# Performance work log

Hardware: AMD Instinct MI355X
Metric: run time of the kernel (lower is better)

Reference implementation:

```python
import jax, jax.numpy as jnp
import numpy as np

GRID_SIZE = 5
SPLINE_ORDER = 3
HIDDEN = 128
N = 131072
K = 256          # num_cluster
EPS = 1e-8       # torch.cosine_similarity eps
N_COEF = GRID_SIZE + SPLINE_ORDER  # 8 spline basis functions per input feature


def make_grid():
    # efficient-kan grid: grid_range [-1,1], extended by spline_order on each side
    h = 2.0 / GRID_SIZE
    g = jnp.arange(-SPLINE_ORDER, GRID_SIZE + SPLINE_ORDER + 1, dtype=jnp.float32) * h - 1.0
    return jnp.tile(g[None, :], (HIDDEN, 1))  # (in, grid_size + 2*order + 1) = (128, 12)


def b_splines(x, grid):
    # x: (N, in), grid: (in, G) -> bases: (N, in, grid_size + spline_order)
    xe = x[..., None]
    bases = ((xe >= grid[:, :-1]) & (xe < grid[:, 1:])).astype(x.dtype)
    for p in range(1, SPLINE_ORDER + 1):
        left = (xe - grid[:, :-(p + 1)]) / (grid[:, p:-1] - grid[:, :-(p + 1)])
        right = (grid[:, p + 1:] - xe) / (grid[:, p + 1:] - grid[:, 1:-p])
        bases = left * bases[..., :-1] + right * bases[..., 1:]
    return bases


def kan_linear(x, grid, base_w, spline_w, scaler):
    # efficient-kan KANLinear: base path + spline path
    base = jax.nn.silu(x) @ base_w.T                       # (N, out)
    sp = b_splines(x, grid)                                # (N, in, coef)
    sw = spline_w * scaler[..., None]                      # (out, in, coef)
    return base + jnp.einsum('nic,oic->no', sp, sw)


def setup_inputs() -> dict:
    key = jax.random.key(0)
    ks = jax.random.split(key, 9)
    s = 1.0 / np.sqrt(HIDDEN)
    return {
        'x': jax.random.normal(ks[0], (N, HIDDEN), jnp.float32),
        'prototypes': jax.random.normal(ks[1], (K, HIDDEN), jnp.float32),
        'grid': make_grid(),
        'base_w1': jax.random.normal(ks[2], (HIDDEN, HIDDEN), jnp.float32) * s,
        'spline_w1': jax.random.normal(ks[3], (HIDDEN, HIDDEN, N_COEF), jnp.float32) * 0.1,
        'scaler1': jax.random.normal(ks[4], (HIDDEN, HIDDEN), jnp.float32) * s + 1.0,
        'base_w2': jax.random.normal(ks[5], (HIDDEN, HIDDEN), jnp.float32) * s,
        'spline_w2': jax.random.normal(ks[6], (HIDDEN, HIDDEN, N_COEF), jnp.float32) * 0.1,
        'scaler2': jax.random.normal(ks[7], (HIDDEN, HIDDEN), jnp.float32) * s + 1.0,
    }


def reference(x, prototypes, grid, base_w1, spline_w1, scaler1, base_w2, spline_w2, scaler2):
    # KAN([128,128,128]) = two KANLinear layers
    h = kan_linear(x, grid, base_w1, spline_w1, scaler1)
    emb = kan_linear(h, grid, base_w2, spline_w2, scaler2)     # (N, 128)
    # cosine similarity to all prototypes = normalized matmul (same math as
    # the broadcasted torch.cosine_similarity, without the (N,K,H) intermediate)
    xn = emb / jnp.maximum(jnp.linalg.norm(emb, axis=-1, keepdims=True), EPS)
    pn = prototypes / jnp.maximum(jnp.linalg.norm(prototypes, axis=-1, keepdims=True), EPS)
    sim = xn @ pn.T                                            # (N, K)
    cluster_assignments = jnp.argmax(sim, axis=1)              # (N,)
    return emb, cluster_assignments
```

## Files before the change

kernel.cpp:

```cpp
#include <hip/hip_runtime.h>
#include <math.h>

typedef unsigned short u16;
typedef _Float16 f16;
typedef __attribute__((ext_vector_type(8))) _Float16 f16x8;
typedef __attribute__((ext_vector_type(4))) float f32x4;

#define N_ROWS 131072
#define HID 128
#define WS_CH 8192
#define N_WCH 72
#define N_PCH 8

__device__ __forceinline__ void f16_split(float v, f16& hi, f16& lo) {
    f16 h = (f16)v;
    hi = h;
    lo = (f16)(v - (float)h);
}

__device__ __forceinline__ void spline8(float xv, float* a8) {
    float s  = (xv + 2.2f) * 2.5f;
    float tf = floorf(s);
    int   tt = (int)tf;
    bool valid = (tt >= 0) && (tt <= 10);
    float kt = (float)(tt - 3) * 0.4f - 1.0f;
    float u  = (xv - kt) * 2.5f;
    float u2 = u * u, u3 = u2 * u;
    float om = 1.0f - u;
    float b3 = u3 * (1.0f / 6.0f);
    float b2 = (-3.f * u3 + 3.f * u2 + 3.f * u + 1.f) * (1.0f / 6.0f);
    float b1 = (3.f * u3 - 6.f * u2 + 4.f) * (1.0f / 6.0f);
    float b0 = om * om * om * (1.0f / 6.0f);
    #pragma unroll
    for (int c = 0; c < 8; ++c) {
        int d = tt - c;
        float v = 0.f;
        v = (d == 0) ? b3 : v;
        v = (d == 1) ? b2 : v;
        v = (d == 2) ? b1 : v;
        v = (d == 3) ? b0 : v;
        a8[c] = valid ? v : 0.f;
    }
}

#define GLOAD_LDS16(g, l)                                                         \
    __builtin_amdgcn_global_load_lds(                                             \
        (const __attribute__((address_space(1))) unsigned int*)(g),               \
        (__attribute__((address_space(3))) unsigned int*)(l), 16, 0, 0)

__global__ __launch_bounds__(256)
void pack_weights(const float* __restrict__ bw1, const float* __restrict__ sw1,
                  const float* __restrict__ sc1,
                  const float* __restrict__ bw2, const float* __restrict__ sw2,
                  const float* __restrict__ sc2,
                  const float* __restrict__ protos, u16* __restrict__ ws)
{
    int gid = blockIdx.x * 256 + threadIdx.x;
    if (gid < N_WCH * 4096) {
        int l  = gid / (36 * 4096);
        int r  = gid % (36 * 4096);
        int ch = r / 4096;
        int e  = r % 4096;
        int o  = e >> 5;
        int kl = e & 31;
        const float* bw = l ? bw2 : bw1;
        const float* sw = l ? sw2 : sw1;
        const float* sc = l ? sc2 : sc1;
        float v;
        if (ch < 4) {
            v = bw[o * HID + ch * 32 + kl];
        } else {
            int i = (ch - 4) * 4 + (kl >> 3);
            v = sw[(o * HID + i) * 8 + (kl & 7)] * sc[o * HID + i];
        }
        f16 hi, lo; f16_split(v, hi, lo);
        int nt = o >> 4, n = o & 15, kq = kl >> 3, c = kl & 7;
        size_t base = (size_t)(l * 36 + ch) * WS_CH;
        size_t idx  = ((size_t)nt * 64 + kq * 16 + n) * 8 + c;
        ws[base + idx]        = __builtin_bit_cast(u16, hi);
        ws[base + 4096 + idx] = __builtin_bit_cast(u16, lo);
    } else if (gid < (N_WCH + N_PCH) * 4096) {
        int r  = gid - N_WCH * 4096;
        int hk = r / 4096;
        int e  = r % 4096;
        int pl = e >> 5;
        int kl = e & 31;
        int half = hk >> 2, kc = hk & 3;
        float v = protos[(size_t)(half * 128 + pl) * HID + kc * 32 + kl];
        f16 hi, lo; f16_split(v, hi, lo);
        int nt = pl >> 4, n = pl & 15, kq = kl >> 3, c = kl & 7;
        size_t base = (size_t)(N_WCH + hk) * WS_CH;
        size_t idx  = ((size_t)nt * 64 + kq * 16 + n) * 8 + c;
        ws[base + idx]        = __builtin_bit_cast(u16, hi);
        ws[base + 4096 + idx] = __builtin_bit_cast(u16, lo);
    }
}

__global__ __launch_bounds__(256, 3)
void kan_fused(const float* __restrict__ x, const float* __restrict__ protos,
               const u16* __restrict__ wpack,
               float* __restrict__ emb_out, float* __restrict__ assign_out)
{
    __shared__ float t[64][132];
    __shared__ u16   Bfrag[2][8][64][8];
    __shared__ float rnp[256];

    const int tid  = threadIdx.x;
    const int lane = tid & 63;
    const int w    = tid >> 6;
    const int m    = lane & 15;
    const int q    = lane >> 4;
    const int row  = w * 16 + m;
    const int brow = blockIdx.x * 64;

    {
        const float4* pr = (const float4*)(protos + (size_t)tid * HID);
        float s = 0.0f;
        #pragma unroll
        for (int j = 0; j < 32; ++j) {
            float4 v = pr[j];
            s += v.x * v.x + v.y * v.y + v.z * v.z + v.w * v.w;
        }
        rnp[tid] = 1.0f / fmaxf(sqrtf(s), 1e-8f);
    }

    {
        const int m2 = tid >> 2, kq2 = tid & 3;
        const float4* src = (const float4*)(x + (size_t)(brow + m2) * HID + kq2 * 32);
        #pragma unroll
        for (int j = 0; j < 8; ++j) {
            float4 v = src[j];
            int k = kq2 * 32 + j * 4;
            t[m2][k] = v.x; t[m2][k + 1] = v.y; t[m2][k + 2] = v.z; t[m2][k + 3] = v.w;
        }
    }
    __syncthreads();

    union { f16x8 v; f16 h[8]; } ah, al, bh, bl;
    f32x4 acc[8];

    for (int l = 0; l < 2; ++l) {
        #pragma unroll
        for (int nt = 0; nt < 8; ++nt) acc[nt] = (f32x4){0.f, 0.f, 0.f, 0.f};

        for (int ch = 0; ch < 36; ++ch) {
            float a8[8];
            if (ch < 4) {
                #pragma unroll
                for (int j = 0; j < 8; ++j) {
                    float xv = t[row][ch * 32 + q * 8 + j];
                    a8[j] = xv / (1.0f + expf(-xv));
                }
            } else {
                spline8(t[row][(ch - 4) * 4 + q], a8);
            }
            #pragma unroll
            for (int j = 0; j < 8; ++j) f16_split(a8[j], ah.h[j], al.h[j]);

            __syncthreads();
            {
                const char* gsrc = (const char*)(wpack + (size_t)(l * 36 + ch) * WS_CH);
                char* lbase = (char*)&Bfrag[0][0][0][0] + w * 4096;
                #pragma unroll
                for (int i = 0; i < 4; ++i)
                    GLOAD_LDS16(gsrc + w * 4096 + i * 1024 + (size_t)lane * 16,
                                lbase + i * 1024);
            }
            __syncthreads();

            #pragma unroll
            for (int nt = 0; nt < 8; ++nt) {
                bh.v = *(const f16x8*)Bfrag[0][nt][lane];
                bl.v = *(const f16x8*)Bfrag[1][nt][lane];
                acc[nt] = __builtin_amdgcn_mfma_f32_16x16x32_f16(ah.v, bh.v, acc[nt], 0, 0, 0);
                acc[nt] = __builtin_amdgcn_mfma_f32_16x16x32_f16(ah.v, bl.v, acc[nt], 0, 0, 0);
                acc[nt] = __builtin_amdgcn_mfma_f32_16x16x32_f16(al.v, bh.v, acc[nt], 0, 0, 0);
                acc[nt] = __builtin_amdgcn_mfma_f32_16x16x32_f16(al.v, bl.v, acc[nt], 0, 0, 0);
            }
        }

        #pragma unroll
        for (int nt = 0; nt < 8; ++nt)
            #pragma unroll
            for (int r = 0; r < 4; ++r)
                t[w * 16 + q * 4 + r][nt * 16 + m] = acc[nt][r];
        __syncthreads();
    }

    {
        const int m2 = tid >> 2, kq2 = tid & 3;
        float* dst = emb_out + (size_t)(brow + m2) * HID + kq2 * 32;
        #pragma unroll
        for (int j = 0; j < 8; ++j)
            *(float4*)(dst + j * 4) = *(const float4*)&t[m2][kq2 * 32 + j * 4];
    }

    float best[4]; int bi[4];
    #pragma unroll
    for (int r = 0; r < 4; ++r) { best[r] = -3.402823466e+38f; bi[r] = 0; }

    for (int half = 0; half < 2; ++half) {
        #pragma unroll
        for (int nt = 0; nt < 8; ++nt) acc[nt] = (f32x4){0.f, 0.f, 0.f, 0.f};

        for (int kc = 0; kc < 4; ++kc) {
            float a8[8];
            #pragma unroll
            for (int j = 0; j < 8; ++j) a8[j] = t[row][kc * 32 + q * 8 + j];
            #pragma unroll
            for (int j = 0; j < 8; ++j) f16_split(a8[j], ah.h[j], al.h[j]);

            __syncthreads();
            {
                const char* gsrc =
                    (const char*)(wpack + (size_t)(N_WCH + half * 4 + kc) * WS_CH);
                char* lbase = (char*)&Bfrag[0][0][0][0] + w * 4096;
                #pragma unroll
                for (int i = 0; i < 4; ++i)
                    GLOAD_LDS16(gsrc + w * 4096 + i * 1024 + (size_t)lane * 16,
                                lbase + i * 1024);
            }
            __syncthreads();

            #pragma unroll
            for (int nt = 0; nt < 8; ++nt) {
                bh.v = *(const f16x8*)Bfrag[0][nt][lane];
                bl.v = *(const f16x8*)Bfrag[1][nt][lane];
                acc[nt] = __builtin_amdgcn_mfma_f32_16x16x32_f16(ah.v, bh.v, acc[nt], 0, 0, 0);
                acc[nt] = __builtin_amdgcn_mfma_f32_16x16x32_f16(ah.v, bl.v, acc[nt], 0, 0, 0);
                acc[nt] = __builtin_amdgcn_mfma_f32_16x16x32_f16(al.v, bh.v, acc[nt], 0, 0, 0);
                acc[nt] = __builtin_amdgcn_mfma_f32_16x16x32_f16(al.v, bl.v, acc[nt], 0, 0, 0);
            }
        }

        #pragma unroll
        for (int nt = 0; nt < 8; ++nt) {
            int p = half * 128 + nt * 16 + m;
            float rp = rnp[p];
            #pragma unroll
            for (int r = 0; r < 4; ++r) {
                float v = acc[nt][r] * rp;
                if (v > best[r]) { best[r] = v; bi[r] = p; }
            }
        }
    }

    #pragma unroll
    for (int r = 0; r < 4; ++r) {
        #pragma unroll
        for (int off = 1; off < 16; off <<= 1) {
            float ov = __shfl_xor(best[r], off);
            int   oi = __shfl_xor(bi[r], off);
            if (ov > best[r] || (ov == best[r] && oi < bi[r])) { best[r] = ov; bi[r] = oi; }
        }
        if (m == 0)
            assign_out[(size_t)brow + w * 16 + q * 4 + r] = (float)bi[r];
    }
}

extern "C" void kernel_launch(void* const* d_in, const int* in_sizes, int n_in,
                              void* d_out, int out_size, void* d_ws, size_t ws_size,
                              hipStream_t stream) {
    (void)in_sizes; (void)n_in; (void)out_size; (void)ws_size;

    const float* x      = (const float*)d_in[0];
    const float* protos = (const float*)d_in[1];
    const float* bw1 = (const float*)d_in[3];
    const float* sw1 = (const float*)d_in[4];
    const float* sc1 = (const float*)d_in[5];
    const float* bw2 = (const float*)d_in[6];
    const float* sw2 = (const float*)d_in[7];
    const float* sc2 = (const float*)d_in[8];

    float* out    = (float*)d_out;
    float* embp   = out;
    float* assign = out + (size_t)N_ROWS * HID;
    u16*   wpack  = (u16*)d_ws;

    pack_weights<<<dim3((N_WCH + N_PCH) * 4096 / 256), dim3(256), 0, stream>>>(
        bw1, sw1, sc1, bw2, sw2, sc2, protos, wpack);
    kan_fused<<<dim3(N_ROWS / 64), dim3(256), 0, stream>>>(
        x, protos, wpack, embp, assign);
}
```

Baseline: 468.7 us.

## Load weight fragments directly from global into registers, drop LDS staging and barriers

```diff
diff --git a/kernel.cpp b/kernel.cpp
--- a/kernel.cpp
+++ b/kernel.cpp
@@ -42,11 +42,6 @@
         a8[c] = valid ? v : 0.f;
     }
 }
-
-#define GLOAD_LDS16(g, l)                                                         \
-    __builtin_amdgcn_global_load_lds(                                             \
-        (const __attribute__((address_space(1))) unsigned int*)(g),               \
-        (__attribute__((address_space(3))) unsigned int*)(l), 16, 0, 0)
 
 __global__ __launch_bounds__(256)
 void pack_weights(const float* __restrict__ bw1, const float* __restrict__ sw1,
@@ -96,13 +91,12 @@
     }
 }
 
-__global__ __launch_bounds__(256, 3)
+__global__ __launch_bounds__(256, 2)
 void kan_fused(const float* __restrict__ x, const float* __restrict__ protos,
                const u16* __restrict__ wpack,
                float* __restrict__ emb_out, float* __restrict__ assign_out)
 {
     __shared__ float t[64][132];
-    __shared__ u16   Bfrag[2][8][64][8];
     __shared__ float rnp[256];
 
     const int tid  = threadIdx.x;
@@ -125,18 +119,19 @@
     }
 
     {
-        const int m2 = tid >> 2, kq2 = tid & 3;
-        const float4* src = (const float4*)(x + (size_t)(brow + m2) * HID + kq2 * 32);
+        const int rl = w * 16 + (lane >> 2);
+        const int kq2 = lane & 3;
+        const float4* src = (const float4*)(x + (size_t)(brow + rl) * HID + kq2 * 32);
         #pragma unroll
         for (int j = 0; j < 8; ++j) {
             float4 v = src[j];
             int k = kq2 * 32 + j * 4;
-            t[m2][k] = v.x; t[m2][k + 1] = v.y; t[m2][k + 2] = v.z; t[m2][k + 3] = v.w;
+            t[rl][k] = v.x; t[rl][k + 1] = v.y; t[rl][k + 2] = v.z; t[rl][k + 3] = v.w;
         }
     }
     __syncthreads();
 
-    union { f16x8 v; f16 h[8]; } ah, al, bh, bl;
+    union { f16x8 v; f16 h[8]; } ah, al;
     f32x4 acc[8];
 
     for (int l = 0; l < 2; ++l) {
@@ -146,36 +141,27 @@
         for (int ch = 0; ch < 36; ++ch) {
             float a8[8];
             if (ch < 4) {
+                float4 xv0 = *(const float4*)&t[row][ch * 32 + q * 8];
+                float4 xv1 = *(const float4*)&t[row][ch * 32 + q * 8 + 4];
+                float xs[8] = { xv0.x, xv0.y, xv0.z, xv0.w, xv1.x, xv1.y, xv1.z, xv1.w };
                 #pragma unroll
-                for (int j = 0; j < 8; ++j) {
-                    float xv = t[row][ch * 32 + q * 8 + j];
-                    a8[j] = xv / (1.0f + expf(-xv));
-                }
+                for (int j = 0; j < 8; ++j)
+                    a8[j] = xs[j] / (1.0f + __expf(-xs[j]));
             } else {
                 spline8(t[row][(ch - 4) * 4 + q], a8);
             }
             #pragma unroll
             for (int j = 0; j < 8; ++j) f16_split(a8[j], ah.h[j], al.h[j]);
 
-            __syncthreads();
-            {
-                const char* gsrc = (const char*)(wpack + (size_t)(l * 36 + ch) * WS_CH);
-                char* lbase = (char*)&Bfrag[0][0][0][0] + w * 4096;
-                #pragma unroll
-                for (int i = 0; i < 4; ++i)
-                    GLOAD_LDS16(gsrc + w * 4096 + i * 1024 + (size_t)lane * 16,
-                                lbase + i * 1024);
-            }
-            __syncthreads();
-
+            const u16* cb = wpack + (size_t)(l * 36 + ch) * WS_CH + (size_t)lane * 8;
             #pragma unroll
             for (int nt = 0; nt < 8; ++nt) {
-                bh.v = *(const f16x8*)Bfrag[0][nt][lane];
-                bl.v = *(const f16x8*)Bfrag[1][nt][lane];
-                acc[nt] = __builtin_amdgcn_mfma_f32_16x16x32_f16(ah.v, bh.v, acc[nt], 0, 0, 0);
-                acc[nt] = __builtin_amdgcn_mfma_f32_16x16x32_f16(ah.v, bl.v, acc[nt], 0, 0, 0);
-                acc[nt] = __builtin_amdgcn_mfma_f32_16x16x32_f16(al.v, bh.v, acc[nt], 0, 0, 0);
-                acc[nt] = __builtin_amdgcn_mfma_f32_16x16x32_f16(al.v, bl.v, acc[nt], 0, 0, 0);
+                f16x8 bh = *(const f16x8*)(cb + nt * 512);
+                f16x8 bl = *(const f16x8*)(cb + 4096 + nt * 512);
+                acc[nt] = __builtin_amdgcn_mfma_f32_16x16x32_f16(ah.v, bh, acc[nt], 0, 0, 0);
+                acc[nt] = __builtin_amdgcn_mfma_f32_16x16x32_f16(ah.v, bl, acc[nt], 0, 0, 0);
+                acc[nt] = __builtin_amdgcn_mfma_f32_16x16x32_f16(al.v, bh, acc[nt], 0, 0, 0);
+                acc[nt] = __builtin_amdgcn_mfma_f32_16x16x32_f16(al.v, bl, acc[nt], 0, 0, 0);
             }
         }
 
@@ -184,15 +170,15 @@
             #pragma unroll
             for (int r = 0; r < 4; ++r)
                 t[w * 16 + q * 4 + r][nt * 16 + m] = acc[nt][r];
-        __syncthreads();
     }
 
     {
-        const int m2 = tid >> 2, kq2 = tid & 3;
-        float* dst = emb_out + (size_t)(brow + m2) * HID + kq2 * 32;
+        const int rl = w * 16 + (lane >> 2);
+        const int kq2 = lane & 3;
+        float* dst = emb_out + (size_t)(brow + rl) * HID + kq2 * 32;
         #pragma unroll
         for (int j = 0; j < 8; ++j)
-            *(float4*)(dst + j * 4) = *(const float4*)&t[m2][kq2 * 32 + j * 4];
+            *(float4*)(dst + j * 4) = *(const float4*)&t[rl][kq2 * 32 + j * 4];
     }
 
     float best[4]; int bi[4];
@@ -204,32 +190,22 @@
         for (int nt = 0; nt < 8; ++nt) acc[nt] = (f32x4){0.f, 0.f, 0.f, 0.f};
 
         for (int kc = 0; kc < 4; ++kc) {
-            float a8[8];
-            #pragma unroll
-            for (int j = 0; j < 8; ++j) a8[j] = t[row][kc * 32 + q * 8 + j];
-            #pragma unroll
-            for (int j = 0; j < 8; ++j) f16_split(a8[j], ah.h[j], al.h[j]);
-
-            __syncthreads();
-            {
-                const char* gsrc =
-                    (const char*)(wpack + (size_t)(N_WCH + half * 4 + kc) * WS_CH);
-                char* lbase = (char*)&Bfrag[0][0][0][0] + w * 4096;
-                #pragma unroll
-                for (int i = 0; i < 4; ++i)
-                    GLOAD_LDS16(gsrc + w * 4096 + i * 1024 + (size_t)lane * 16,
-                                lbase + i * 1024);
-            }
-            __syncthreads();
-
+            float4 ev0 = *(const float4*)&t[row][kc * 32 + q * 8];
+            float4 ev1 = *(const float4*)&t[row][kc * 32 + q * 8 + 4];
+            float es[8] = { ev0.x, ev0.y, ev0.z, ev0.w, ev1.x, ev1.y, ev1.z, ev1.w };
+            #pragma unroll
+            for (int j = 0; j < 8; ++j) f16_split(es[j], ah.h[j], al.h[j]);
+
+            const u16* cb = wpack + (size_t)(N_WCH + half * 4 + kc) * WS_CH
+                          + (size_t)lane * 8;
             #pragma unroll
             for (int nt = 0; nt < 8; ++nt) {
-                bh.v = *(const f16x8*)Bfrag[0][nt][lane];
-                bl.v = *(const f16x8*)Bfrag[1][nt][lane];
-                acc[nt] = __builtin_amdgcn_mfma_f32_16x16x32_f16(ah.v, bh.v, acc[nt], 0, 0, 0);
-                acc[nt] = __builtin_amdgcn_mfma_f32_16x16x32_f16(ah.v, bl.v, acc[nt], 0, 0, 0);
-                acc[nt] = __builtin_amdgcn_mfma_f32_16x16x32_f16(al.v, bh.v, acc[nt], 0, 0, 0);
-                acc[nt] = __builtin_amdgcn_mfma_f32_16x16x32_f16(al.v, bl.v, acc[nt], 0, 0, 0);
+                f16x8 bh = *(const f16x8*)(cb + nt * 512);
+                f16x8 bl = *(const f16x8*)(cb + 4096 + nt * 512);
+                acc[nt] = __builtin_amdgcn_mfma_f32_16x16x32_f16(ah.v, bh, acc[nt], 0, 0, 0);
+                acc[nt] = __builtin_amdgcn_mfma_f32_16x16x32_f16(ah.v, bl, acc[nt], 0, 0, 0);
+                acc[nt] = __builtin_amdgcn_mfma_f32_16x16x32_f16(al.v, bh, acc[nt], 0, 0, 0);
+                acc[nt] = __builtin_amdgcn_mfma_f32_16x16x32_f16(al.v, bl, acc[nt], 0, 0, 0);
             }
         }
 
```

After: 639.9 us. +36.5%, slower.
